# Performance work log

Hardware: AMD Instinct MI355X
Metric: run time of the kernel (lower is better)

## Reference

```python
import jax, jax.numpy as jnp
import numpy as np

B, T, S, E, H, V = 64, 32, 64, 128, 256, 32000


def setup_inputs() -> dict:
    key = jax.random.key(0)
    ks = jax.random.split(key, 13)
    n = lambda k, sh, s=1.0: jax.random.normal(k, sh, dtype=jnp.float32) * s
    return {
        "target": n(ks[0], (B, T, E)),
        "inp": n(ks[1], (B, T, E)),
        "pos_feature": n(ks[2], (B, E)),
        "encoder_state": n(ks[3], (B, H)),
        "encoder_output": n(ks[4], (B, S, 2 * H)),
        "W_ih": n(ks[5], (3 * H, 3 * E + H), 0.05),
        "W_hh": n(ks[6], (3 * H, H), 0.05),
        "b_ih": n(ks[7], (3 * H,), 0.05),
        "b_hh": n(ks[8], (3 * H,), 0.05),
        "Win_w": n(ks[9], (2 * H, H), 0.05),
        "Win_b": n(ks[10], (2 * H,), 0.05),
        "Wout_w": n(ks[11], (V, 3 * H), 0.05),
        "Wout_b": n(ks[12], (V,), 0.05),
    }


def reference(target, inp, pos_feature, encoder_state, encoder_output,
              W_ih, W_hh, b_ih, b_hh, Win_w, Win_b, Wout_w, Wout_b):
    bsz = target.shape[0]
    hdim = W_hh.shape[1]

    def gru_cell(x, h):
        gi = x @ W_ih.T + b_ih          # [B, 3H]
        gh = h @ W_hh.T + b_hh          # [B, 3H]
        i_r, i_z, i_n = jnp.split(gi, 3, axis=1)
        h_r, h_z, h_n = jnp.split(gh, 3, axis=1)
        r = jax.nn.sigmoid(i_r + h_r)
        z = jax.nn.sigmoid(i_z + h_z)
        n = jnp.tanh(i_n + r * h_n)
        return (1.0 - z) * n + z * h

    def step(hs, xs):
        dec_in, in_t = xs                                   # [B,E], [B,E]
        x = jnp.concatenate([dec_in, pos_feature, encoder_state, in_t], axis=1)
        hs = gru_cell(x, hs)
        q = hs @ Win_w.T + Win_b                            # [B, 2H]
        attn = jnp.einsum('bsd,bd->bs', encoder_output, q)  # [B, S]
        score = jax.nn.softmax(attn, axis=1)
        h_star = jnp.einsum('bs,bsd->bd', score, encoder_output)  # [B, 2H]
        feat = jnp.concatenate([h_star, hs], axis=1)        # [B, 3H]
        out = jax.nn.log_softmax(jax.nn.relu(feat @ Wout_w.T + Wout_b), axis=1)
        return hs, out

    hs0 = jnp.zeros((bsz, hdim), dtype=target.dtype)
    xs = (jnp.swapaxes(target, 0, 1), jnp.swapaxes(inp, 0, 1))  # time-major
    hs, outputs = jax.lax.scan(step, hs0, xs)
    return hs, outputs  # hs: [B,H], outputs: [T,B,V]
```

## Files before the change

### kernel.cpp

```cpp
#include <hip/hip_runtime.h>
#include <hip/hip_bf16.h>


typedef __attribute__((ext_vector_type(8))) short  s8v;
typedef __attribute__((ext_vector_type(8))) __bf16 bf8v;
typedef __attribute__((ext_vector_type(4))) float  f4v;
typedef __attribute__((ext_vector_type(2))) float  f2v;

#define DEV static __device__ __forceinline__

DEV ushort f2b(float f) {
  unsigned u = __float_as_uint(f);
  u += 0x7fffu + ((u >> 16) & 1u);
  return (ushort)(u >> 16);
}
DEV float b2fs(short s) { return __uint_as_float(((unsigned)(ushort)s) << 16); }

__global__ __launch_bounds__(256) void k_gather(
    const float* __restrict__ target, const float* __restrict__ inp,
    const float* __restrict__ posf,   const float* __restrict__ encs,
    ushort* __restrict__ X) {
  int tb = blockIdx.x; int t = tb >> 6, b = tb & 63;
  size_t xrow = (size_t)tb * 640;
  for (int c = threadIdx.x; c < 640; c += 256) {
    float v;
    if (c < 128)      v = target[((size_t)b * 32 + t) * 128 + c];
    else if (c < 256) v = posf[(size_t)b * 128 + (c - 128)];
    else if (c < 512) v = encs[(size_t)b * 256 + (c - 256)];
    else              v = inp[((size_t)b * 32 + t) * 128 + (c - 512)];
    X[xrow + c] = f2b(v);
  }
}

template <bool RELU>
__global__ __launch_bounds__(256) void k_gemm_bt(
    const ushort* __restrict__ A, const float* __restrict__ B,
    const float* __restrict__ bias, float* __restrict__ Out,
    int N, int K) {
  __shared__ __align__(16) ushort As[128 * 40];
  __shared__ __align__(16) ushort Bs[128 * 40];
  const int m0 = blockIdx.x * 128, n0 = blockIdx.y * 128;
  const int tid = threadIdx.x;
  const int lane = tid & 63, wv = tid >> 6;
  const int wm = (wv >> 1) * 64, wn = (wv & 1) * 64;
  const int fr = lane & 15, fq = lane >> 4;
  const int srow = tid >> 2, scol = (tid & 3) * 8;
  f4v acc[4][4];
#pragma unroll
  for (int i = 0; i < 4; ++i)
#pragma unroll
    for (int j = 0; j < 4; ++j) acc[i][j] = {0.f, 0.f, 0.f, 0.f};
  const ushort* ag = A + (size_t)(m0 + srow) * K + scol;
  const float*  bg = B + (size_t)(n0 + srow) * K + scol;
  for (int k0 = 0; k0 < K; k0 += 32) {
    s8v a0 = *(const s8v*)(ag + k0);
    s8v a1 = *(const s8v*)(ag + k0 + (size_t)64 * K);
    f4v b00 = *(const f4v*)(bg + k0);
    f4v b01 = *(const f4v*)(bg + k0 + 4);
    f4v b10 = *(const f4v*)(bg + k0 + (size_t)64 * K);
    f4v b11 = *(const f4v*)(bg + k0 + (size_t)64 * K + 4);
    s8v b0, b1;
#pragma unroll
    for (int u = 0; u < 4; ++u) {
      b0[u]     = (short)f2b(b00[u]);
      b0[u + 4] = (short)f2b(b01[u]);
      b1[u]     = (short)f2b(b10[u]);
      b1[u + 4] = (short)f2b(b11[u]);
    }
    __syncthreads();
    *(s8v*)&As[srow * 40 + scol] = a0;
    *(s8v*)&As[(srow + 64) * 40 + scol] = a1;
    *(s8v*)&Bs[srow * 40 + scol] = b0;
    *(s8v*)&Bs[(srow + 64) * 40 + scol] = b1;
    __syncthreads();
    bf8v af[4], bfr[4];
#pragma unroll
    for (int i = 0; i < 4; ++i)
      af[i] = *(const bf8v*)&As[(wm + i * 16 + fr) * 40 + fq * 8];
#pragma unroll
    for (int j = 0; j < 4; ++j)
      bfr[j] = *(const bf8v*)&Bs[(wn + j * 16 + fr) * 40 + fq * 8];
#pragma unroll
    for (int i = 0; i < 4; ++i)
#pragma unroll
      for (int j = 0; j < 4; ++j)
        acc[i][j] = __builtin_amdgcn_mfma_f32_16x16x32_bf16(af[i], bfr[j],
                                                            acc[i][j], 0, 0, 0);
  }
  float bj[4];
#pragma unroll
  for (int j = 0; j < 4; ++j) bj[j] = bias[n0 + wn + j * 16 + fr];
#pragma unroll
  for (int i = 0; i < 4; ++i) {
#pragma unroll
    for (int j = 0; j < 4; ++j) {
#pragma unroll
      for (int r = 0; r < 4; ++r) {
        int gm = m0 + wm + i * 16 + fq * 4 + r;
        int gn = n0 + wn + j * 16 + fr;
        float v = acc[i][j][r] + bj[j];
        if (RELU) v = fmaxf(v, 0.f);
        Out[(size_t)gm * N + gn] = v;
      }
    }
  }
}

__global__ __launch_bounds__(1024) void k_recur(
    const float* __restrict__ gi_all,
    const float* __restrict__ eo,
    const float* __restrict__ Whh,
    const float* __restrict__ bhh,
    const float* __restrict__ Winw,
    const float* __restrict__ Winb,
    ushort* __restrict__ feat,
    float* __restrict__ hs_out) {
  const int b = blockIdx.x, tid = threadIdx.x;
  __shared__ __align__(16) float h[256];
  __shared__ __align__(16) float q[512];
  __shared__ float attnp[64];
  __shared__ float score[64];
  const float* eoB = eo + (size_t)b * 32768;

  const int t = tid >> 2, p = tid & 3;
  const float* wr = Whh + (size_t)t * 256 + p * 4;
  const float* wz = wr + 65536;
  const float* wn = wr + 131072;
  const float bhr = bhh[t], bhz = bhh[t + 256], bhn = bhh[t + 512];

  const int qo = tid >> 1, qp = tid & 1;
  const float* wq = Winw + (size_t)qo * 256 + qp * 4;
  const float qb = Winb[qo];

  const int as = tid >> 4, aj = tid & 15;

  if (tid < 256) h[tid] = 0.f;
  __syncthreads();

  for (int st = 0; st < 32; ++st) {
    const float* gi = gi_all + ((size_t)st * 64 + b) * 768;
    float g0 = gi[t], g1 = gi[t + 256], g2 = gi[t + 512];
    float ar = 0.f, az = 0.f, an = 0.f;
#pragma unroll
    for (int i = 0; i < 16; ++i) {
      f4v hv = *(const f4v*)&h[p * 4 + i * 16];
      f4v rv = *(const f4v*)(wr + i * 16);
      f4v zv = *(const f4v*)(wz + i * 16);
      f4v nv = *(const f4v*)(wn + i * 16);
#pragma unroll
      for (int u = 0; u < 4; ++u) {
        ar = fmaf(hv[u], rv[u], ar);
        az = fmaf(hv[u], zv[u], az);
        an = fmaf(hv[u], nv[u], an);
      }
    }
    ar += __shfl_xor(ar, 1); ar += __shfl_xor(ar, 2);
    az += __shfl_xor(az, 1); az += __shfl_xor(az, 2);
    an += __shfl_xor(an, 1); an += __shfl_xor(an, 2);
    float hnew = 0.f;
    if (p == 0) {
      float r = 1.f / (1.f + __expf(-(g0 + ar + bhr)));
      float z = 1.f / (1.f + __expf(-(g1 + az + bhz)));
      float e2 = __expf(2.f * (g2 + r * (an + bhn)));
      float n = 1.f - 2.f / (e2 + 1.f);
      hnew = (1.f - z) * n + z * h[t];
    }
    __syncthreads();
    if (p == 0) h[t] = hnew;
    __syncthreads();
    float a0 = 0.f, a1 = 0.f;
#pragma unroll
    for (int i = 0; i < 32; i += 2) {
      f4v h0 = *(const f4v*)&h[qp * 4 + i * 8];
      f4v w0 = *(const f4v*)(wq + i * 8);
      f4v h1 = *(const f4v*)&h[qp * 4 + i * 8 + 8];
      f4v w1 = *(const f4v*)(wq + i * 8 + 8);
#pragma unroll
      for (int u = 0; u < 4; ++u) {
        a0 = fmaf(h0[u], w0[u], a0);
        a1 = fmaf(h1[u], w1[u], a1);
      }
    }
    a0 += a1;
    a0 += __shfl_xor(a0, 1);
    if (qp == 0) q[qo] = a0 + qb;
    __syncthreads();
    float aa = 0.f;
#pragma unroll
    for (int i = 0; i < 8; ++i) {
      int kk = aj * 4 + i * 64;
      f4v ev = *(const f4v*)(eoB + (size_t)as * 512 + kk);
      f4v qv = *(const f4v*)&q[kk];
#pragma unroll
      for (int u = 0; u < 4; ++u) aa = fmaf(ev[u], qv[u], aa);
    }
    aa += __shfl_xor(aa, 1); aa += __shfl_xor(aa, 2);
    aa += __shfl_xor(aa, 4); aa += __shfl_xor(aa, 8);
    if (aj == 0) attnp[as] = aa;
    __syncthreads();
    if (tid < 64) {
      float a = attnp[tid];
      float m = a;
#pragma unroll
      for (int off = 32; off > 0; off >>= 1) m = fmaxf(m, __shfl_xor(m, off));
      float e = __expf(a - m);
      float ss = e;
#pragma unroll
      for (int off = 32; off > 0; off >>= 1) ss += __shfl_xor(ss, off);
      score[tid] = e / ss;
    }
    __syncthreads();
    size_t row = ((size_t)st * 64 + b) * 768;
    {
      int d0 = 2 * t;
      float s0 = 0.f, s1 = 0.f;
#pragma unroll
      for (int i = 0; i < 16; ++i) {
        int s2 = p * 16 + i;
        float sc = score[s2];
        f2v ev = *(const f2v*)(eoB + (size_t)s2 * 512 + d0);
        s0 = fmaf(sc, ev.x, s0);
        s1 = fmaf(sc, ev.y, s1);
      }
      s0 += __shfl_xor(s0, 1); s0 += __shfl_xor(s0, 2);
      s1 += __shfl_xor(s1, 1); s1 += __shfl_xor(s1, 2);
      if (p == 0) {
        feat[row + d0] = f2b(s0);
        feat[row + d0 + 1] = f2b(s1);
      }
    }
    if (tid < 256) feat[row + 512 + tid] = f2b(h[tid]);
  }
  if (tid < 256) hs_out[(size_t)b * 256 + tid] = h[tid];
}

__global__ __launch_bounds__(256) void k_logsm(float* __restrict__ out) {
  float* p = out + (size_t)blockIdx.x * 32000;
  const int t = threadIdx.x;
  __shared__ float red[4];
  float m = 0.f;
  for (int c = t; c < 4000; c += 256) {
    f4v a = *(const f4v*)(p + (size_t)c * 8);
    f4v b = *(const f4v*)(p + (size_t)c * 8 + 4);
    m = fmaxf(m, fmaxf(fmaxf(a.x, a.y), fmaxf(a.z, a.w)));
    m = fmaxf(m, fmaxf(fmaxf(b.x, b.y), fmaxf(b.z, b.w)));
  }
#pragma unroll
  for (int off = 32; off > 0; off >>= 1) m = fmaxf(m, __shfl_xor(m, off));
  if ((t & 63) == 0) red[t >> 6] = m;
  __syncthreads();
  m = fmaxf(fmaxf(red[0], red[1]), fmaxf(red[2], red[3]));
  float s = 0.f;
  for (int c = t; c < 4000; c += 256) {
    f4v a = *(const f4v*)(p + (size_t)c * 8);
    f4v b = *(const f4v*)(p + (size_t)c * 8 + 4);
    s += __expf(a.x - m) + __expf(a.y - m) + __expf(a.z - m) + __expf(a.w - m);
    s += __expf(b.x - m) + __expf(b.y - m) + __expf(b.z - m) + __expf(b.w - m);
  }
#pragma unroll
  for (int off = 32; off > 0; off >>= 1) s += __shfl_xor(s, off);
  __syncthreads();
  if ((t & 63) == 0) red[t >> 6] = s;
  __syncthreads();
  s = red[0] + red[1] + red[2] + red[3];
  const float L = m + logf(s);
  for (int c = t; c < 4000; c += 256) {
    f4v a = *(const f4v*)(p + (size_t)c * 8);
    f4v b = *(const f4v*)(p + (size_t)c * 8 + 4);
    a.x -= L; a.y -= L; a.z -= L; a.w -= L;
    b.x -= L; b.y -= L; b.z -= L; b.w -= L;
    *(f4v*)(p + (size_t)c * 8) = a;
    *(f4v*)(p + (size_t)c * 8 + 4) = b;
  }
}

extern "C" void kernel_launch(void* const* d_in, const int* in_sizes, int n_in,
                              void* d_out, int out_size, void* d_ws, size_t ws_size,
                              hipStream_t stream) {
  (void)in_sizes; (void)n_in; (void)out_size; (void)ws_size;
  const float* target = (const float*)d_in[0];
  const float* inp    = (const float*)d_in[1];
  const float* posf   = (const float*)d_in[2];
  const float* encs   = (const float*)d_in[3];
  const float* enco   = (const float*)d_in[4];
  const float* Wih    = (const float*)d_in[5];
  const float* Whh    = (const float*)d_in[6];
  const float* bih    = (const float*)d_in[7];
  const float* bhh    = (const float*)d_in[8];
  const float* Winw   = (const float*)d_in[9];
  const float* Winb   = (const float*)d_in[10];
  const float* Woutw  = (const float*)d_in[11];
  const float* Woutb  = (const float*)d_in[12];

  char* ws = (char*)d_ws;
  ushort* X    = (ushort*)(ws);
  float*  gi   = (float*)(ws + 0x300000);
  ushort* feat = (ushort*)(ws + 0x900000);
  float* hs    = (float*)d_out;
  float* logits = hs + 16384;

  k_gather<<<2048, 256, 0, stream>>>(target, inp, posf, encs, X);
  k_gemm_bt<false><<<dim3(16, 6), 256, 0, stream>>>(X, Wih, bih, gi, 768, 640);
  k_recur<<<64, 1024, 0, stream>>>(gi, enco, Whh, bhh, Winw, Winb, feat, hs);
  k_gemm_bt<true><<<dim3(16, 250), 256, 0, stream>>>(feat, Woutw, Woutb, logits,
                                                     32000, 768);
  k_logsm<<<2048, 256, 0, stream>>>(logits);
}
```

Before: 2.011 ms.

## Batch four sequences per recurrence block to reuse W_hh and Win loads

The recurrent kernel now handles four batch elements per 1024-thread block, with 16 blocks instead of 64. Each W_hh and Win weight load from global memory is reused across four hidden states, cutting weight traffic per step by four. The gate math is spread across all four lanes instead of only lane 0, and the attention and context loops are reorganised per batch. The cost is fewer blocks (16 CUs busy), more registers per thread, and a longer serial context loop per thread.

```diff
diff --git a/kernel.cpp b/kernel.cpp
--- a/kernel.cpp
+++ b/kernel.cpp
@@ -106,7 +106,7 @@
   }
 }
 
-__global__ __launch_bounds__(1024) void k_recur(
+__global__ __launch_bounds__(1024, 4) void k_recur(
     const float* __restrict__ gi_all,
     const float* __restrict__ eo,
     const float* __restrict__ Whh,
@@ -115,91 +115,125 @@
     const float* __restrict__ Winb,
     ushort* __restrict__ feat,
     float* __restrict__ hs_out) {
-  const int b = blockIdx.x, tid = threadIdx.x;
-  __shared__ __align__(16) float h[256];
-  __shared__ __align__(16) float q[512];
-  __shared__ float attnp[64];
-  __shared__ float score[64];
-  const float* eoB = eo + (size_t)b * 32768;
+  const int b4 = blockIdx.x * 4, tid = threadIdx.x;
+  __shared__ __align__(16) float h[4][256];
+  __shared__ __align__(16) float q[4][512];
+  __shared__ float attnp[4][64];
+  __shared__ float score[4][64];
 
   const int t = tid >> 2, p = tid & 3;
   const float* wr = Whh + (size_t)t * 256 + p * 4;
   const float* wz = wr + 65536;
   const float* wn = wr + 131072;
   const float bhr = bhh[t], bhz = bhh[t + 256], bhn = bhh[t + 512];
+  const float* giT = gi_all + (size_t)(b4 + p) * 768 + t;
 
   const int qo = tid >> 1, qp = tid & 1;
   const float* wq = Winw + (size_t)qo * 256 + qp * 4;
   const float qb = Winb[qo];
 
-  const int as = tid >> 4, aj = tid & 15;
-
-  if (tid < 256) h[tid] = 0.f;
+  const int ab = tid >> 8, as = (tid >> 2) & 63, ap = tid & 3;
+  const float* eoA = eo + (size_t)(b4 + ab) * 32768 + as * 512 + ap * 128;
+
+  const int hb = tid >> 8, hd = tid & 255;
+  const float* eoH = eo + (size_t)(b4 + hb) * 32768 + 2 * hd;
+
+  h[tid >> 8][tid & 255] = 0.f;
   __syncthreads();
 
   for (int st = 0; st < 32; ++st) {
-    const float* gi = gi_all + ((size_t)st * 64 + b) * 768;
-    float g0 = gi[t], g1 = gi[t + 256], g2 = gi[t + 512];
-    float ar = 0.f, az = 0.f, an = 0.f;
+    float g0 = giT[(size_t)st * 49152];
+    float g1 = giT[(size_t)st * 49152 + 256];
+    float g2 = giT[(size_t)st * 49152 + 512];
+    float hold = h[p][t];
+    float ar0 = 0, ar1 = 0, ar2 = 0, ar3 = 0;
+    float az0 = 0, az1 = 0, az2 = 0, az3 = 0;
+    float an0 = 0, an1 = 0, an2 = 0, an3 = 0;
 #pragma unroll
     for (int i = 0; i < 16; ++i) {
-      f4v hv = *(const f4v*)&h[p * 4 + i * 16];
       f4v rv = *(const f4v*)(wr + i * 16);
       f4v zv = *(const f4v*)(wz + i * 16);
       f4v nv = *(const f4v*)(wn + i * 16);
+      f4v h0 = *(const f4v*)&h[0][p * 4 + i * 16];
+      f4v h1 = *(const f4v*)&h[1][p * 4 + i * 16];
+      f4v h2 = *(const f4v*)&h[2][p * 4 + i * 16];
+      f4v h3 = *(const f4v*)&h[3][p * 4 + i * 16];
 #pragma unroll
       for (int u = 0; u < 4; ++u) {
-        ar = fmaf(hv[u], rv[u], ar);
-        az = fmaf(hv[u], zv[u], az);
-        an = fmaf(hv[u], nv[u], an);
-      }
-    }
-    ar += __shfl_xor(ar, 1); ar += __shfl_xor(ar, 2);
-    az += __shfl_xor(az, 1); az += __shfl_xor(az, 2);
-    an += __shfl_xor(an, 1); an += __shfl_xor(an, 2);
-    float hnew = 0.f;
-    if (p == 0) {
-      float r = 1.f / (1.f + __expf(-(g0 + ar + bhr)));
-      float z = 1.f / (1.f + __expf(-(g1 + az + bhz)));
-      float e2 = __expf(2.f * (g2 + r * (an + bhn)));
-      float n = 1.f - 2.f / (e2 + 1.f);
-      hnew = (1.f - z) * n + z * h[t];
-    }
-    __syncthreads();
-    if (p == 0) h[t] = hnew;
-    __syncthreads();
-    float a0 = 0.f, a1 = 0.f;
-#pragma unroll
-    for (int i = 0; i < 32; i += 2) {
-      f4v h0 = *(const f4v*)&h[qp * 4 + i * 8];
-      f4v w0 = *(const f4v*)(wq + i * 8);
-      f4v h1 = *(const f4v*)&h[qp * 4 + i * 8 + 8];
-      f4v w1 = *(const f4v*)(wq + i * 8 + 8);
+        ar0 = fmaf(h0[u], rv[u], ar0); az0 = fmaf(h0[u], zv[u], az0); an0 = fmaf(h0[u], nv[u], an0);
+        ar1 = fmaf(h1[u], rv[u], ar1); az1 = fmaf(h1[u], zv[u], az1); an1 = fmaf(h1[u], nv[u], an1);
+        ar2 = fmaf(h2[u], rv[u], ar2); az2 = fmaf(h2[u], zv[u], az2); an2 = fmaf(h2[u], nv[u], an2);
+        ar3 = fmaf(h3[u], rv[u], ar3); az3 = fmaf(h3[u], zv[u], az3); an3 = fmaf(h3[u], nv[u], an3);
+      }
+    }
+    ar0 += __shfl_xor(ar0, 1); ar0 += __shfl_xor(ar0, 2);
+    ar1 += __shfl_xor(ar1, 1); ar1 += __shfl_xor(ar1, 2);
+    ar2 += __shfl_xor(ar2, 1); ar2 += __shfl_xor(ar2, 2);
+    ar3 += __shfl_xor(ar3, 1); ar3 += __shfl_xor(ar3, 2);
+    az0 += __shfl_xor(az0, 1); az0 += __shfl_xor(az0, 2);
+    az1 += __shfl_xor(az1, 1); az1 += __shfl_xor(az1, 2);
+    az2 += __shfl_xor(az2, 1); az2 += __shfl_xor(az2, 2);
+    az3 += __shfl_xor(az3, 1); az3 += __shfl_xor(az3, 2);
+    an0 += __shfl_xor(an0, 1); an0 += __shfl_xor(an0, 2);
+    an1 += __shfl_xor(an1, 1); an1 += __shfl_xor(an1, 2);
+    an2 += __shfl_xor(an2, 1); an2 += __shfl_xor(an2, 2);
+    an3 += __shfl_xor(an3, 1); an3 += __shfl_xor(an3, 2);
+    float arS = p == 0 ? ar0 : p == 1 ? ar1 : p == 2 ? ar2 : ar3;
+    float azS = p == 0 ? az0 : p == 1 ? az1 : p == 2 ? az2 : az3;
+    float anS = p == 0 ? an0 : p == 1 ? an1 : p == 2 ? an2 : an3;
+    float r = 1.f / (1.f + __expf(-(g0 + arS + bhr)));
+    float z = 1.f / (1.f + __expf(-(g1 + azS + bhz)));
+    float e2 = __expf(2.f * (g2 + r * (anS + bhn)));
+    float n = 1.f - 2.f / (e2 + 1.f);
+    float hnew = (1.f - z) * n + z * hold;
+    __syncthreads();
+    h[p][t] = hnew;
+    feat[((size_t)st * 64 + b4 + p) * 768 + 512 + t] = f2b(hnew);
+    __syncthreads();
+    float a0 = 0, a1 = 0, a2 = 0, a3 = 0;
+#pragma unroll
+    for (int i = 0; i < 32; ++i) {
+      f4v wv = *(const f4v*)(wq + i * 8);
+      f4v h0 = *(const f4v*)&h[0][qp * 4 + i * 8];
+      f4v h1 = *(const f4v*)&h[1][qp * 4 + i * 8];
+      f4v h2 = *(const f4v*)&h[2][qp * 4 + i * 8];
+      f4v h3 = *(const f4v*)&h[3][qp * 4 + i * 8];
 #pragma unroll
       for (int u = 0; u < 4; ++u) {
-        a0 = fmaf(h0[u], w0[u], a0);
-        a1 = fmaf(h1[u], w1[u], a1);
-      }
-    }
-    a0 += a1;
+        a0 = fmaf(h0[u], wv[u], a0);
+        a1 = fmaf(h1[u], wv[u], a1);
+        a2 = fmaf(h2[u], wv[u], a2);
+        a3 = fmaf(h3[u], wv[u], a3);
+      }
+    }
     a0 += __shfl_xor(a0, 1);
-    if (qp == 0) q[qo] = a0 + qb;
-    __syncthreads();
-    float aa = 0.f;
-#pragma unroll
-    for (int i = 0; i < 8; ++i) {
-      int kk = aj * 4 + i * 64;
-      f4v ev = *(const f4v*)(eoB + (size_t)as * 512 + kk);
-      f4v qv = *(const f4v*)&q[kk];
-#pragma unroll
-      for (int u = 0; u < 4; ++u) aa = fmaf(ev[u], qv[u], aa);
-    }
-    aa += __shfl_xor(aa, 1); aa += __shfl_xor(aa, 2);
-    aa += __shfl_xor(aa, 4); aa += __shfl_xor(aa, 8);
-    if (aj == 0) attnp[as] = aa;
-    __syncthreads();
-    if (tid < 64) {
-      float a = attnp[tid];
+    a1 += __shfl_xor(a1, 1);
+    a2 += __shfl_xor(a2, 1);
+    a3 += __shfl_xor(a3, 1);
+    if (qp == 0) { q[0][qo] = a0 + qb; q[2][qo] = a2 + qb; }
+    else         { q[1][qo] = a1 + qb; q[3][qo] = a3 + qb; }
+    __syncthreads();
+    {
+      float aa0 = 0.f, aa1 = 0.f;
+      const float* qv = &q[ab][ap * 128];
+#pragma unroll
+      for (int i = 0; i < 16; ++i) {
+        f4v e0 = *(const f4v*)(eoA + i * 8);
+        f4v e1 = *(const f4v*)(eoA + i * 8 + 4);
+        f4v q0 = *(const f4v*)(qv + i * 8);
+        f4v q1 = *(const f4v*)(qv + i * 8 + 4);
+        aa0 = fmaf(e0.x, q0.x, aa0); aa0 = fmaf(e0.y, q0.y, aa0);
+        aa0 = fmaf(e0.z, q0.z, aa0); aa0 = fmaf(e0.w, q0.w, aa0);
+        aa1 = fmaf(e1.x, q1.x, aa1); aa1 = fmaf(e1.y, q1.y, aa1);
+        aa1 = fmaf(e1.z, q1.z, aa1); aa1 = fmaf(e1.w, q1.w, aa1);
+      }
+      float aa = aa0 + aa1;
+      aa += __shfl_xor(aa, 1); aa += __shfl_xor(aa, 2);
+      if (ap == 0) attnp[ab][as] = aa;
+    }
+    __syncthreads();
+    if (tid < 256) {
+      float a = attnp[tid >> 6][tid & 63];
       float m = a;
 #pragma unroll
       for (int off = 32; off > 0; off >>= 1) m = fmaxf(m, __shfl_xor(m, off));
@@ -207,31 +241,24 @@
       float ss = e;
 #pragma unroll
       for (int off = 32; off > 0; off >>= 1) ss += __shfl_xor(ss, off);
-      score[tid] = e / ss;
-    }
-    __syncthreads();
-    size_t row = ((size_t)st * 64 + b) * 768;
+      score[tid >> 6][tid & 63] = e / ss;
+    }
+    __syncthreads();
     {
-      int d0 = 2 * t;
       float s0 = 0.f, s1 = 0.f;
-#pragma unroll
-      for (int i = 0; i < 16; ++i) {
-        int s2 = p * 16 + i;
-        float sc = score[s2];
-        f2v ev = *(const f2v*)(eoB + (size_t)s2 * 512 + d0);
+#pragma unroll 8
+      for (int s2 = 0; s2 < 64; ++s2) {
+        float sc = score[hb][s2];
+        f2v ev = *(const f2v*)(eoH + (size_t)s2 * 512);
         s0 = fmaf(sc, ev.x, s0);
         s1 = fmaf(sc, ev.y, s1);
       }
-      s0 += __shfl_xor(s0, 1); s0 += __shfl_xor(s0, 2);
-      s1 += __shfl_xor(s1, 1); s1 += __shfl_xor(s1, 2);
-      if (p == 0) {
-        feat[row + d0] = f2b(s0);
-        feat[row + d0 + 1] = f2b(s1);
-      }
-    }
-    if (tid < 256) feat[row + 512 + tid] = f2b(h[tid]);
-  }
-  if (tid < 256) hs_out[(size_t)b * 256 + tid] = h[tid];
+      size_t row = ((size_t)st * 64 + b4 + hb) * 768;
+      feat[row + 2 * hd] = f2b(s0);
+      feat[row + 2 * hd + 1] = f2b(s1);
+    }
+  }
+  hs_out[(size_t)(b4 + (tid >> 8)) * 256 + (tid & 255)] = h[tid >> 8][tid & 255];
 }
 
 __global__ __launch_bounds__(256) void k_logsm(float* __restrict__ out) {
@@ -301,7 +328,7 @@
 
   k_gather<<<2048, 256, 0, stream>>>(target, inp, posf, encs, X);
   k_gemm_bt<false><<<dim3(16, 6), 256, 0, stream>>>(X, Wih, bih, gi, 768, 640);
-  k_recur<<<64, 1024, 0, stream>>>(gi, enco, Whh, bhh, Winw, Winb, feat, hs);
+  k_recur<<<16, 1024, 0, stream>>>(gi, enco, Whh, bhh, Winw, Winb, feat, hs);
   k_gemm_bt<true><<<dim3(16, 250), 256, 0, stream>>>(feat, Woutw, Woutb, logits,
                                                      32000, 768);
   k_logsm<<<2048, 256, 0, stream>>>(logits);
```

New measurement: 2.856 ms. +42.0%, slower.
